# Performance work log

Measured on AMD Instinct MI355X. Metric: run time of the kernel, lower is better.

## Reference

```python
import jax, jax.numpy as jnp
import numpy as np

MEM_CLIP = 3.0   # memory_cell_clip_value
STATE_CLIP = 3.0 # state_projection_clip_value

L, DIRS = 2, 2
B, T, D = 64, 128, 512
H, C = 512, 4096


def _run_direction(x, Wi, Wh, b, Wp, reverse):
    """One ElmoLstmCell (LSTM w/ projection + clipping) over time.
    x: [B,T,Din]; Wi: [4C,Din]; Wh: [4C,H]; b: [4C]; Wp: [H,C].
    Returns outputs [B,T,H], final h [B,H], final c [B,C]."""
    Bsz = x.shape[0]
    cdim = Wi.shape[0] // 4
    hdim = Wp.shape[0]
    h0 = jnp.zeros((Bsz, hdim), x.dtype)
    c0 = jnp.zeros((Bsz, cdim), x.dtype)
    xs = jnp.swapaxes(x, 0, 1)  # [T,B,Din]

    def step(carry, xt):
        h, c = carry
        gates = xt @ Wi.T + h @ Wh.T + b  # [B,4C]
        i, f, g, o = jnp.split(gates, 4, axis=-1)
        i = jax.nn.sigmoid(i)
        f = jax.nn.sigmoid(f)
        g = jnp.tanh(g)
        o = jax.nn.sigmoid(o)
        c_new = jnp.clip(i * g + f * c, -MEM_CLIP, MEM_CLIP)
        h_new = jnp.clip((o * jnp.tanh(c_new)) @ Wp.T, -STATE_CLIP, STATE_CLIP)
        return (h_new, c_new), h_new

    (hT, cT), ys = jax.lax.scan(step, (h0, c0), xs, reverse=reverse)
    return jnp.swapaxes(ys, 0, 1), hT, cT


def setup_inputs() -> dict:
    key = jax.random.key(0)
    ks = jax.random.split(key, 5)
    x = jax.random.normal(ks[0], (B, T, D), jnp.float32)
    Wi = jax.random.normal(ks[1], (L, DIRS, 4 * C, D), jnp.float32) / np.sqrt(D)
    Wh = jax.random.normal(ks[2], (L, DIRS, 4 * C, H), jnp.float32) / np.sqrt(H)
    b = jax.random.normal(ks[3], (L, DIRS, 4 * C), jnp.float32) * 0.01
    Wp = jax.random.normal(ks[4], (L, DIRS, H, C), jnp.float32) / np.sqrt(C)
    return {"x": x, "Wi": Wi, "Wh": Wh, "b": b, "Wp": Wp}


def reference(x, Wi, Wh, b, Wp):
    nlayers = Wi.shape[0]
    fwd_in, bwd_in = x, x
    seq_outs, hs, cs = [], [], []
    for l in range(nlayers):
        f_out, fh, fc = _run_direction(fwd_in, Wi[l, 0], Wh[l, 0], b[l, 0], Wp[l, 0], reverse=False)
        b_out, bh, bc = _run_direction(bwd_in, Wi[l, 1], Wh[l, 1], b[l, 1], Wp[l, 1], reverse=True)
        if l != 0:  # highway/residual between stacked layers
            f_out = f_out + fwd_in
            b_out = b_out + bwd_in
        fwd_in, bwd_in = f_out, b_out
        seq_outs.append(jnp.concatenate([f_out, b_out], axis=-1))  # [B,T,2H]
        hs.append(jnp.concatenate([fh, bh], axis=-1))               # [B,2H]
        cs.append(jnp.concatenate([fc, bc], axis=-1))               # [B,2C]
    return jnp.stack(seq_outs), jnp.stack(hs), jnp.stack(cs)
```

## Files before the change

### kernel.cpp

```cpp
#include <hip/hip_runtime.h>
#include <hip/hip_bf16.h>
#include <stdint.h>
#include <math.h>


#define BB 64
#define TT 128
#define DD 512
#define HH 512
#define CC 4096

typedef __bf16 v8bf __attribute__((ext_vector_type(8)));
typedef float  v4f  __attribute__((ext_vector_type(4)));
typedef short  v8s  __attribute__((ext_vector_type(8)));

__device__ __forceinline__ uint16_t f2bf(float f) {
    unsigned int x = __float_as_uint(f);
    unsigned int r = (x + 0x7fffu + ((x >> 16) & 1u)) >> 16;
    return (uint16_t)r;
}
__device__ __forceinline__ float sigm(float x) { return 1.0f / (1.0f + __expf(-x)); }

__global__ __launch_bounds__(256) void k_conv_wfull(
        const float* __restrict__ Wi, const float* __restrict__ Wh,
        uint16_t* __restrict__ Wf) {
    size_t i   = (size_t)blockIdx.x * blockDim.x + threadIdx.x;
    size_t idx = i * 8;
    size_t row = idx >> 10;
    int    k   = (int)(idx & 1023);
    const float* s = (k < 512) ? (Wh + row * 512 + k) : (Wi + row * 512 + (k - 512));
    float4 f0 = ((const float4*)s)[0];
    float4 f1 = ((const float4*)s)[1];
    v8s v;
    v[0]=f2bf(f0.x); v[1]=f2bf(f0.y); v[2]=f2bf(f0.z); v[3]=f2bf(f0.w);
    v[4]=f2bf(f1.x); v[5]=f2bf(f1.y); v[6]=f2bf(f1.z); v[7]=f2bf(f1.w);
    ((v8s*)Wf)[i] = v;
}

__global__ __launch_bounds__(256) void k_conv_plain(
        const float* __restrict__ src, uint16_t* __restrict__ dst, int n8) {
    int i = blockIdx.x * blockDim.x + threadIdx.x;
    if (i >= n8) return;
    const float4* s = (const float4*)(src + (size_t)i * 8);
    float4 f0 = s[0];
    float4 f1 = s[1];
    v8s v;
    v[0]=f2bf(f0.x); v[1]=f2bf(f0.y); v[2]=f2bf(f0.z); v[3]=f2bf(f0.w);
    v[4]=f2bf(f1.x); v[5]=f2bf(f1.y); v[6]=f2bf(f1.z); v[7]=f2bf(f1.w);
    ((v8s*)dst)[i] = v;
}

__global__ __launch_bounds__(256) void k_gates(
        const uint16_t* __restrict__ Wl,
        const float*    __restrict__ bl,
        const uint16_t* __restrict__ hprev,
        const uint16_t* __restrict__ xs0,
        const uint16_t* __restrict__ xs1,
        float*    __restrict__ c_state,
        uint16_t* __restrict__ act,
        float*    __restrict__ cs_out,
        int t_step, int flags) {
    const int dir  = blockIdx.y;
    const int bx   = blockIdx.x;
    const int tid  = threadIdx.x;
    const int w    = tid >> 6;
    const int lane = tid & 63;
    const int col  = lane & 15;
    const int quad = lane >> 4;
    const int tt   = dir ? (127 - t_step) : t_step;
    const bool first = (flags & 1), last = (flags & 2);

    const uint16_t* xsrc = dir ? xs1 : xs0;
    const uint16_t* hp   = hprev + (size_t)dir * BB * HH;
    const uint16_t* Wd   = Wl + (size_t)dir * 16384 * 1024;

    v4f acc[4][2] = {};
    const uint16_t* brow[2];
#pragma unroll
    for (int nt = 0; nt < 2; ++nt) {
        int j = w * 4096 + bx * 32 + nt * 16 + col;
        brow[nt] = Wd + (size_t)j * 1024;
    }

    int ks0 = first ? 16 : 0;
    for (int ks = ks0; ks < 32; ++ks) {
        int k = ks * 32 + quad * 8;
        v8bf a[4], bf[2];
        if (k < 512) {
#pragma unroll
            for (int mt = 0; mt < 4; ++mt) {
                int m = mt * 16 + col;
                a[mt] = *(const v8bf*)(hp + (size_t)m * HH + k);
            }
        } else {
#pragma unroll
            for (int mt = 0; mt < 4; ++mt) {
                int m = mt * 16 + col;
                a[mt] = *(const v8bf*)(xsrc + ((size_t)m * TT + tt) * DD + (k - 512));
            }
        }
#pragma unroll
        for (int nt = 0; nt < 2; ++nt) bf[nt] = *(const v8bf*)(brow[nt] + k);
#pragma unroll
        for (int mt = 0; mt < 4; ++mt)
#pragma unroll
            for (int nt = 0; nt < 2; ++nt)
                acc[mt][nt] = __builtin_amdgcn_mfma_f32_16x16x32_bf16(
                        a[mt], bf[nt], acc[mt][nt], 0, 0, 0);
    }

    __shared__ float gt[4][64][33];
#pragma unroll
    for (int mt = 0; mt < 4; ++mt)
#pragma unroll
        for (int nt = 0; nt < 2; ++nt)
#pragma unroll
            for (int r = 0; r < 4; ++r)
                gt[w][mt * 16 + quad * 4 + r][nt * 16 + col] = acc[mt][nt][r];
    __syncthreads();

    const float* bd = bl + (size_t)dir * 16384;
#pragma unroll
    for (int i = 0; i < 8; ++i) {
        int idx  = i * 256 + tid;
        int m    = idx >> 5;
        int cl   = idx & 31;
        int cell = bx * 32 + cl;
        float xi = gt[0][m][cl] + bd[cell];
        float xf = gt[1][m][cl] + bd[4096 + cell];
        float xg = gt[2][m][cl] + bd[8192 + cell];
        float xo = gt[3][m][cl] + bd[12288 + cell];
        float iv = sigm(xi), fv = sigm(xf), ov = sigm(xo);
        float gv = tanhf(xg);
        size_t cidx = ((size_t)dir * BB + m) * CC + cell;
        float cold = first ? 0.0f : c_state[cidx];
        float cn = fminf(fmaxf(iv * gv + fv * cold, -3.0f), 3.0f);
        c_state[cidx] = cn;
        act[cidx] = f2bf(ov * tanhf(cn));
        if (last) cs_out[(size_t)m * 8192 + dir * 4096 + cell] = cn;
    }
}

__global__ __launch_bounds__(256) void k_proj(
        const uint16_t* __restrict__ Wpl,
        const uint16_t* __restrict__ act,
        uint16_t* __restrict__ hout,
        uint16_t* __restrict__ hseq,
        float* __restrict__ seq_out,
        const float* __restrict__ resid,
        float* __restrict__ hs_out,
        int t_step, int last) {
    const int bn   = blockIdx.x;
    const int bm   = blockIdx.y;
    const int dir  = blockIdx.z;
    const int tid  = threadIdx.x;
    const int w    = tid >> 6;
    const int lane = tid & 63;
    const int col  = lane & 15;
    const int quad = lane >> 4;
    const int tt   = dir ? (127 - t_step) : t_step;

    const uint16_t* A  = act + ((size_t)dir * BB + bm * 16 + col) * CC;
    const uint16_t* Br = Wpl + ((size_t)dir * HH + bn * 16 + col) * CC;

    v4f acc = {};
#pragma unroll 8
    for (int ks = w * 32; ks < w * 32 + 32; ++ks) {
        int k = ks * 32 + quad * 8;
        v8bf a  = *(const v8bf*)(A + k);
        v8bf bb = *(const v8bf*)(Br + k);
        acc = __builtin_amdgcn_mfma_f32_16x16x32_bf16(a, bb, acc, 0, 0, 0);
    }
    __shared__ float red[4][256];
#pragma unroll
    for (int r = 0; r < 4; ++r)
        red[w][(quad * 4 + r) * 16 + col] = acc[r];
    __syncthreads();

    int e = tid;
    float s = red[0][e] + red[1][e] + red[2][e] + red[3][e];
    float h = fminf(fmaxf(s, -3.0f), 3.0f);
    int ml = e >> 4, nl = e & 15;
    int m = bm * 16 + ml, n = bn * 16 + nl;
    uint16_t hb = f2bf(h);
    hout[((size_t)dir * BB + m) * HH + n] = hb;
    if (hseq) hseq[(((size_t)dir * BB + m) * TT + tt) * HH + n] = hb;
    size_t so = ((size_t)m * TT + tt) * 1024 + (size_t)dir * 512 + n;
    float outv = h;
    if (resid) outv += resid[so];
    seq_out[so] = outv;
    if (last) hs_out[(size_t)m * 1024 + dir * 512 + n] = h;
}

extern "C" void kernel_launch(void* const* d_in, const int* in_sizes, int n_in,
                              void* d_out, int out_size, void* d_ws, size_t ws_size,
                              hipStream_t stream) {
    const float* x  = (const float*)d_in[0];
    const float* Wi = (const float*)d_in[1];
    const float* Wh = (const float*)d_in[2];
    const float* bb = (const float*)d_in[3];
    const float* Wp = (const float*)d_in[4];
    float* out = (float*)d_out;

    char* ws = (char*)d_ws;
    size_t off = 0;
    auto take = [&](size_t bytes) -> char* {
        char* p = ws + off;
        off = (off + bytes + 255) & ~(size_t)255;
        return p;
    };
    uint16_t* Wf   = (uint16_t*)take(2ull * 2 * 16384 * 1024 * 2);
    uint16_t* Wpb  = (uint16_t*)take(2ull * 2 * 512 * 4096 * 2);
    uint16_t* xb   = (uint16_t*)take((size_t)BB * TT * DD * 2);
    uint16_t* hseq = (uint16_t*)take(2ull * BB * TT * HH * 2);
    uint16_t* hb   = (uint16_t*)take(2ull * BB * HH * 2);
    uint16_t* actb = (uint16_t*)take(2ull * BB * CC * 2);
    float*    cst  = (float*)take(2ull * BB * CC * 4);

    hipLaunchKernelGGL(k_conv_wfull, dim3(32768), dim3(256), 0, stream, Wi, Wh, Wf);
    hipLaunchKernelGGL(k_conv_plain, dim3(4096), dim3(256), 0, stream, Wp, Wpb,
                       2 * 2 * 512 * 4096 / 8);
    hipLaunchKernelGGL(k_conv_plain, dim3(2048), dim3(256), 0, stream, x, xb,
                       BB * TT * DD / 8);

    const size_t SEQ = (size_t)BB * TT * 1024;
    float* hs_base = out + 2 * SEQ;
    float* cs_base = hs_base + 2ull * BB * 1024;

    for (int l = 0; l < 2; ++l) {
        const uint16_t* Wl  = Wf + (size_t)l * 2 * 16384 * 1024;
        const float*    blp = bb + (size_t)l * 2 * 16384;
        const uint16_t* Wpl = Wpb + (size_t)l * 2 * 512 * 4096;
        const uint16_t* xs0 = l ? hseq : xb;
        const uint16_t* xs1 = l ? hseq + (size_t)BB * TT * HH : xb;
        float* seq_l = out + (size_t)l * SEQ;
        float* cs_l  = cs_base + (size_t)l * BB * 8192;
        float* hs_l  = hs_base + (size_t)l * BB * 1024;
        for (int t = 0; t < TT; ++t) {
            int flags = (t == 0 ? 1 : 0) | (t == TT - 1 ? 2 : 0);
            hipLaunchKernelGGL(k_gates, dim3(128, 2), dim3(256), 0, stream,
                               Wl, blp, hb, xs0, xs1, cst, actb, cs_l, t, flags);
            hipLaunchKernelGGL(k_proj, dim3(32, 4, 2), dim3(256), 0, stream,
                               Wpl, actb, hb,
                               (l == 0) ? hseq : (uint16_t*)nullptr,
                               seq_l,
                               (l == 1) ? (const float*)out : (const float*)nullptr,
                               hs_l, t, (t == TT - 1) ? 1 : 0);
        }
    }
}
```

Measured before the change: 10.90 ms.

## Fuse recurrent steps into one persistent cooperative kernel with grid barriers

Replaces 512 per-timestep launches of the gate and projection kernels with a single persistent cooperative kernel of 256 blocks. Each block keeps its slice of the gate weights in registers for the whole layer and its projection-weight tile in swizzled LDS, and keeps the cell state in registers instead of global memory. Timesteps are separated by software grid barriers built on atomics. This removes launch overhead and repeated weight reloads, but needs very high register and LDS use, one block per CU, and co-residency of all blocks for the barrier to be safe.

```diff
diff --git a/kernel.cpp b/kernel.cpp
--- a/kernel.cpp
+++ b/kernel.cpp
@@ -9,6 +9,8 @@
 #define DD 512
 #define HH 512
 #define CC 4096
+#define NBLK 256
+#define LDS_BYTES 147968
 
 typedef __bf16 v8bf __attribute__((ext_vector_type(8)));
 typedef float  v4f  __attribute__((ext_vector_type(4)));
@@ -50,146 +52,178 @@
     ((v8s*)dst)[i] = v;
 }
 
-__global__ __launch_bounds__(256) void k_gates(
-        const uint16_t* __restrict__ Wl,
-        const float*    __restrict__ bl,
-        const uint16_t* __restrict__ hprev,
-        const uint16_t* __restrict__ xs0,
-        const uint16_t* __restrict__ xs1,
-        float*    __restrict__ c_state,
-        uint16_t* __restrict__ act,
-        float*    __restrict__ cs_out,
-        int t_step, int flags) {
-    const int dir  = blockIdx.y;
-    const int bx   = blockIdx.x;
+__global__ __launch_bounds__(256) void k_init(uint16_t* __restrict__ hbuf,
+                                              unsigned* __restrict__ bar) {
+    int idx = blockIdx.x * 256 + threadIdx.x;
+    if (idx < 8192) ((int4*)hbuf)[idx] = make_int4(0, 0, 0, 0);
+    if (blockIdx.x == 0 && threadIdx.x < 64) bar[threadIdx.x] = 0;
+}
+
+__device__ __forceinline__ void gridbar(unsigned* cnt, unsigned* gen) {
+    __syncthreads();
+    if (threadIdx.x == 0) {
+        unsigned g = __hip_atomic_load(gen, __ATOMIC_RELAXED, __HIP_MEMORY_SCOPE_AGENT);
+        unsigned a = __hip_atomic_fetch_add(cnt, 1u, __ATOMIC_ACQ_REL, __HIP_MEMORY_SCOPE_AGENT);
+        if (a == NBLK - 1u) {
+            __hip_atomic_store(cnt, 0u, __ATOMIC_RELAXED, __HIP_MEMORY_SCOPE_AGENT);
+            __hip_atomic_fetch_add(gen, 1u, __ATOMIC_ACQ_REL, __HIP_MEMORY_SCOPE_AGENT);
+        } else {
+            while (__hip_atomic_load(gen, __ATOMIC_RELAXED, __HIP_MEMORY_SCOPE_AGENT) == g)
+                __builtin_amdgcn_s_sleep(2);
+            __builtin_amdgcn_fence(__ATOMIC_ACQUIRE, "agent");
+        }
+    }
+    __syncthreads();
+}
+
+__global__ __launch_bounds__(256, 1) void k_elmo(
+        const uint16_t* __restrict__ Wf,
+        const float*    __restrict__ bias,
+        const uint16_t* __restrict__ Wpb,
+        const uint16_t* __restrict__ xb,
+        uint16_t* __restrict__ hseq,
+        uint16_t* __restrict__ hbuf,
+        uint16_t* __restrict__ actb,
+        float*    __restrict__ out,
+        unsigned* __restrict__ bar) {
     const int tid  = threadIdx.x;
     const int w    = tid >> 6;
     const int lane = tid & 63;
     const int col  = lane & 15;
     const int quad = lane >> 4;
-    const int tt   = dir ? (127 - t_step) : t_step;
-    const bool first = (flags & 1), last = (flags & 2);
-
-    const uint16_t* xsrc = dir ? xs1 : xs0;
-    const uint16_t* hp   = hprev + (size_t)dir * BB * HH;
-    const uint16_t* Wd   = Wl + (size_t)dir * 16384 * 1024;
-
-    v4f acc[4][2] = {};
-    const uint16_t* brow[2];
-#pragma unroll
-    for (int nt = 0; nt < 2; ++nt) {
-        int j = w * 4096 + bx * 32 + nt * 16 + col;
-        brow[nt] = Wd + (size_t)j * 1024;
+    const int bx   = blockIdx.x;
+    const int gdir = bx >> 7, cellblk = bx & 127;
+    const int xcd  = bx & 7,  rr = bx >> 3;
+    const int pdir = xcd >> 2, pbm = xcd & 3, pbn = rr;
+
+    __shared__ __attribute__((aligned(128))) char lds[LDS_BYTES];
+    float (*gt)[32][33] = (float (*)[32][33])(lds + 131072);
+    float* red = (float*)(lds + 131072);
+
+    unsigned* cnt = bar;
+    unsigned* gen = bar + 32;
+
+    const size_t SEQ = (size_t)BB * TT * 1024;
+    float* hs_base = out + 2 * SEQ;
+    float* cs_base = hs_base + 2ull * BB * 1024;
+
+    float c_reg[8];
+    v8bf  wreg[2][32];
+
+    for (int l = 0; l < 2; ++l) {
+        const uint16_t* Wl   = Wf + (size_t)l * 2 * 16384 * 1024;
+        const float*    bd   = bias + ((size_t)l * 2 + gdir) * 16384;
+        const uint16_t* Wpl  = Wpb + ((size_t)l * 2 + pdir) * 512 * 4096;
+        const uint16_t* xsrc = l ? (hseq + (size_t)gdir * BB * TT * HH) : xb;
+        float* seq_l = out + (size_t)l * SEQ;
+        float* hs_l  = hs_base + (size_t)l * BB * 1024;
+        float* cs_l  = cs_base + (size_t)l * BB * 8192;
+
+#pragma unroll
+        for (int nt = 0; nt < 2; ++nt) {
+            int j = w * 4096 + cellblk * 32 + nt * 16 + col;
+            const uint16_t* rp = Wl + ((size_t)gdir * 16384 + j) * 1024 + quad * 8;
+#pragma unroll
+            for (int ks = 0; ks < 32; ++ks)
+                wreg[nt][ks] = *(const v8bf*)(rp + ks * 32);
+        }
+        for (int c8 = tid; c8 < 8192; c8 += 256) {
+            int row = c8 >> 9;
+            int off = (c8 & 511) << 4;
+            const uint16_t* src = Wpl + (size_t)(pbn * 16 + row) * 4096 + (off >> 1);
+            v8s v = *(const v8s*)src;
+            *(v8s*)(lds + ((row * 8192 + off) ^ ((row & 7) << 4))) = v;
+        }
+        __syncthreads();
+
+        for (int t = 0; t < TT; ++t) {
+            const bool first = (t == 0), last = (t == TT - 1);
+            const int gtt = gdir ? (TT - 1 - t) : t;
+
+            v4f acc[4][2] = {};
+            const uint16_t* hA = hbuf + (size_t)gdir * BB * HH;
+#pragma unroll
+            for (int ks = 0; ks < 32; ++ks) {
+                v8bf a[4];
+                if (ks < 16) {
+                    int k = ks * 32 + quad * 8;
+#pragma unroll
+                    for (int mt = 0; mt < 4; ++mt)
+                        a[mt] = *(const v8bf*)(hA + (size_t)(mt * 16 + col) * HH + k);
+                } else {
+                    int k = (ks - 16) * 32 + quad * 8;
+#pragma unroll
+                    for (int mt = 0; mt < 4; ++mt)
+                        a[mt] = *(const v8bf*)(xsrc + ((size_t)(mt * 16 + col) * TT + gtt) * DD + k);
+                }
+#pragma unroll
+                for (int mt = 0; mt < 4; ++mt)
+#pragma unroll
+                    for (int nt = 0; nt < 2; ++nt)
+                        acc[mt][nt] = __builtin_amdgcn_mfma_f32_16x16x32_bf16(
+                                a[mt], wreg[nt][ks], acc[mt][nt], 0, 0, 0);
+            }
+
+#pragma unroll
+            for (int p = 0; p < 2; ++p) {
+#pragma unroll
+                for (int mh = 0; mh < 2; ++mh)
+#pragma unroll
+                    for (int nt = 0; nt < 2; ++nt)
+#pragma unroll
+                        for (int r = 0; r < 4; ++r)
+                            gt[w][mh * 16 + quad * 4 + r][nt * 16 + col] = acc[p * 2 + mh][nt][r];
+                __syncthreads();
+#pragma unroll
+                for (int i = 0; i < 4; ++i) {
+                    int idx  = i * 256 + tid;
+                    int mloc = idx >> 5, cl = idx & 31;
+                    int m    = p * 32 + mloc;
+                    int cell = cellblk * 32 + cl;
+                    float xi = gt[0][mloc][cl] + bd[cell];
+                    float xf = gt[1][mloc][cl] + bd[4096 + cell];
+                    float xg = gt[2][mloc][cl] + bd[8192 + cell];
+                    float xo = gt[3][mloc][cl] + bd[12288 + cell];
+                    float iv = sigm(xi), fv = sigm(xf), ov = sigm(xo);
+                    float gv = tanhf(xg);
+                    float cold = first ? 0.0f : c_reg[p * 4 + i];
+                    float cn = fminf(fmaxf(iv * gv + fv * cold, -3.0f), 3.0f);
+                    c_reg[p * 4 + i] = cn;
+                    actb[((size_t)gdir * BB + m) * CC + cell] = f2bf(ov * tanhf(cn));
+                    if (last) cs_l[(size_t)m * 8192 + gdir * 4096 + cell] = cn;
+                }
+                __syncthreads();
+            }
+
+            gridbar(cnt, gen);
+
+            const int ptt = pdir ? (TT - 1 - t) : t;
+            const uint16_t* Arow = actb + ((size_t)pdir * BB + pbm * 16 + col) * CC + quad * 8;
+            v4f pacc = {};
+#pragma unroll
+            for (int ki = 0; ki < 32; ++ki) {
+                int ks = w * 32 + ki;
+                v8bf a = *(const v8bf*)(Arow + (size_t)ks * 32);
+                int byte = (col * 8192 + ks * 64 + quad * 16) ^ ((col & 7) << 4);
+                v8bf b = *(const v8bf*)(lds + byte);
+                pacc = __builtin_amdgcn_mfma_f32_16x16x32_bf16(a, b, pacc, 0, 0, 0);
+            }
+#pragma unroll
+            for (int r = 0; r < 4; ++r)
+                red[w * 256 + (quad * 4 + r) * 16 + col] = pacc[r];
+            __syncthreads();
+            float s = red[tid] + red[256 + tid] + red[512 + tid] + red[768 + tid];
+            float h = fminf(fmaxf(s, -3.0f), 3.0f);
+            int m = pbm * 16 + (tid >> 4), n = pbn * 16 + (tid & 15);
+            hbuf[((size_t)pdir * BB + m) * HH + n] = last ? (uint16_t)0 : f2bf(h);
+            if (l == 0) hseq[(((size_t)pdir * BB + m) * TT + ptt) * HH + n] = f2bf(h);
+            size_t so = ((size_t)m * TT + ptt) * 1024 + (size_t)pdir * 512 + n;
+            seq_l[so] = l ? (h + out[so]) : h;
+            if (last) hs_l[(size_t)m * 1024 + pdir * 512 + n] = h;
+
+            gridbar(cnt, gen);
+        }
     }
-
-    int ks0 = first ? 16 : 0;
-    for (int ks = ks0; ks < 32; ++ks) {
-        int k = ks * 32 + quad * 8;
-        v8bf a[4], bf[2];
-        if (k < 512) {
-#pragma unroll
-            for (int mt = 0; mt < 4; ++mt) {
-                int m = mt * 16 + col;
-                a[mt] = *(const v8bf*)(hp + (size_t)m * HH + k);
-            }
-        } else {
-#pragma unroll
-            for (int mt = 0; mt < 4; ++mt) {
-                int m = mt * 16 + col;
-                a[mt] = *(const v8bf*)(xsrc + ((size_t)m * TT + tt) * DD + (k - 512));
-            }
-        }
-#pragma unroll
-        for (int nt = 0; nt < 2; ++nt) bf[nt] = *(const v8bf*)(brow[nt] + k);
-#pragma unroll
-        for (int mt = 0; mt < 4; ++mt)
-#pragma unroll
-            for (int nt = 0; nt < 2; ++nt)
-                acc[mt][nt] = __builtin_amdgcn_mfma_f32_16x16x32_bf16(
-                        a[mt], bf[nt], acc[mt][nt], 0, 0, 0);
-    }
-
-    __shared__ float gt[4][64][33];
-#pragma unroll
-    for (int mt = 0; mt < 4; ++mt)
-#pragma unroll
-        for (int nt = 0; nt < 2; ++nt)
-#pragma unroll
-            for (int r = 0; r < 4; ++r)
-                gt[w][mt * 16 + quad * 4 + r][nt * 16 + col] = acc[mt][nt][r];
-    __syncthreads();
-
-    const float* bd = bl + (size_t)dir * 16384;
-#pragma unroll
-    for (int i = 0; i < 8; ++i) {
-        int idx  = i * 256 + tid;
-        int m    = idx >> 5;
-        int cl   = idx & 31;
-        int cell = bx * 32 + cl;
-        float xi = gt[0][m][cl] + bd[cell];
-        float xf = gt[1][m][cl] + bd[4096 + cell];
-        float xg = gt[2][m][cl] + bd[8192 + cell];
-        float xo = gt[3][m][cl] + bd[12288 + cell];
-        float iv = sigm(xi), fv = sigm(xf), ov = sigm(xo);
-        float gv = tanhf(xg);
-        size_t cidx = ((size_t)dir * BB + m) * CC + cell;
-        float cold = first ? 0.0f : c_state[cidx];
-        float cn = fminf(fmaxf(iv * gv + fv * cold, -3.0f), 3.0f);
-        c_state[cidx] = cn;
-        act[cidx] = f2bf(ov * tanhf(cn));
-        if (last) cs_out[(size_t)m * 8192 + dir * 4096 + cell] = cn;
-    }
-}
-
-__global__ __launch_bounds__(256) void k_proj(
-        const uint16_t* __restrict__ Wpl,
-        const uint16_t* __restrict__ act,
-        uint16_t* __restrict__ hout,
-        uint16_t* __restrict__ hseq,
-        float* __restrict__ seq_out,
-        const float* __restrict__ resid,
-        float* __restrict__ hs_out,
-        int t_step, int last) {
-    const int bn   = blockIdx.x;
-    const int bm   = blockIdx.y;
-    const int dir  = blockIdx.z;
-    const int tid  = threadIdx.x;
-    const int w    = tid >> 6;
-    const int lane = tid & 63;
-    const int col  = lane & 15;
-    const int quad = lane >> 4;
-    const int tt   = dir ? (127 - t_step) : t_step;
-
-    const uint16_t* A  = act + ((size_t)dir * BB + bm * 16 + col) * CC;
-    const uint16_t* Br = Wpl + ((size_t)dir * HH + bn * 16 + col) * CC;
-
-    v4f acc = {};
-#pragma unroll 8
-    for (int ks = w * 32; ks < w * 32 + 32; ++ks) {
-        int k = ks * 32 + quad * 8;
-        v8bf a  = *(const v8bf*)(A + k);
-        v8bf bb = *(const v8bf*)(Br + k);
-        acc = __builtin_amdgcn_mfma_f32_16x16x32_bf16(a, bb, acc, 0, 0, 0);
-    }
-    __shared__ float red[4][256];
-#pragma unroll
-    for (int r = 0; r < 4; ++r)
-        red[w][(quad * 4 + r) * 16 + col] = acc[r];
-    __syncthreads();
-
-    int e = tid;
-    float s = red[0][e] + red[1][e] + red[2][e] + red[3][e];
-    float h = fminf(fmaxf(s, -3.0f), 3.0f);
-    int ml = e >> 4, nl = e & 15;
-    int m = bm * 16 + ml, n = bn * 16 + nl;
-    uint16_t hb = f2bf(h);
-    hout[((size_t)dir * BB + m) * HH + n] = hb;
-    if (hseq) hseq[(((size_t)dir * BB + m) * TT + tt) * HH + n] = hb;
-    size_t so = ((size_t)m * TT + tt) * 1024 + (size_t)dir * 512 + n;
-    float outv = h;
-    if (resid) outv += resid[so];
-    seq_out[so] = outv;
-    if (last) hs_out[(size_t)m * 1024 + dir * 512 + n] = h;
 }
 
 extern "C" void kernel_launch(void* const* d_in, const int* in_sizes, int n_in,
@@ -213,39 +247,28 @@
     uint16_t* Wpb  = (uint16_t*)take(2ull * 2 * 512 * 4096 * 2);
     uint16_t* xb   = (uint16_t*)take((size_t)BB * TT * DD * 2);
     uint16_t* hseq = (uint16_t*)take(2ull * BB * TT * HH * 2);
-    uint16_t* hb   = (uint16_t*)take(2ull * BB * HH * 2);
+    uint16_t* hbuf = (uint16_t*)take(2ull * BB * HH * 2);
     uint16_t* actb = (uint16_t*)take(2ull * BB * CC * 2);
-    float*    cst  = (float*)take(2ull * BB * CC * 4);
+    unsigned* bar  = (unsigned*)take(256);
 
     hipLaunchKernelGGL(k_conv_wfull, dim3(32768), dim3(256), 0, stream, Wi, Wh, Wf);
     hipLaunchKernelGGL(k_conv_plain, dim3(4096), dim3(256), 0, stream, Wp, Wpb,
                        2 * 2 * 512 * 4096 / 8);
     hipLaunchKernelGGL(k_conv_plain, dim3(2048), dim3(256), 0, stream, x, xb,
                        BB * TT * DD / 8);
-
-    const size_t SEQ = (size_t)BB * TT * 1024;
-    float* hs_base = out + 2 * SEQ;
-    float* cs_base = hs_base + 2ull * BB * 1024;
-
-    for (int l = 0; l < 2; ++l) {
-        const uint16_t* Wl  = Wf + (size_t)l * 2 * 16384 * 1024;
-        const float*    blp = bb + (size_t)l * 2 * 16384;
-        const uint16_t* Wpl = Wpb + (size_t)l * 2 * 512 * 4096;
-        const uint16_t* xs0 = l ? hseq : xb;
-        const uint16_t* xs1 = l ? hseq + (size_t)BB * TT * HH : xb;
-        float* seq_l = out + (size_t)l * SEQ;
-        float* cs_l  = cs_base + (size_t)l * BB * 8192;
-        float* hs_l  = hs_base + (size_t)l * BB * 1024;
-        for (int t = 0; t < TT; ++t) {
-            int flags = (t == 0 ? 1 : 0) | (t == TT - 1 ? 2 : 0);
-            hipLaunchKernelGGL(k_gates, dim3(128, 2), dim3(256), 0, stream,
-                               Wl, blp, hb, xs0, xs1, cst, actb, cs_l, t, flags);
-            hipLaunchKernelGGL(k_proj, dim3(32, 4, 2), dim3(256), 0, stream,
-                               Wpl, actb, hb,
-                               (l == 0) ? hseq : (uint16_t*)nullptr,
-                               seq_l,
-                               (l == 1) ? (const float*)out : (const float*)nullptr,
-                               hs_l, t, (t == TT - 1) ? 1 : 0);
-        }
+    hipLaunchKernelGGL(k_init, dim3(32), dim3(256), 0, stream, hbuf, bar);
+
+    const uint16_t* Wf_c  = Wf;
+    const float*    bb_c  = bb;
+    const uint16_t* Wpb_c = Wpb;
+    const uint16_t* xb_c  = xb;
+    void* args[] = { (void*)&Wf_c, (void*)&bb_c, (void*)&Wpb_c, (void*)&xb_c,
+                     (void*)&hseq, (void*)&hbuf, (void*)&actb, (void*)&out,
+                     (void*)&bar };
+    hipError_t e = hipLaunchCooperativeKernel((const void*)k_elmo, dim3(NBLK),
+                                              dim3(256), args, 0, stream);
+    if (e != hipSuccess) {
+        hipLaunchKernelGGL(k_elmo, dim3(NBLK), dim3(256), 0, stream,
+                           Wf_c, bb_c, Wpb_c, xb_c, hseq, hbuf, actb, out, bar);
     }
 }
```

Result: slower. 14.27 ms (+30.9%).
